# Optimization experiments

Hardware: AMD Instinct MI355X
Metric: run time of the kernel (lower is better)

## Reference

```python
import jax, jax.numpy as jnp
import numpy as np

B, S, D, H = 2, 2048, 1024, 16
HD = D // H


def setup_inputs() -> dict:
    key = jax.random.key(0)
    ks = jax.random.split(key, 9)
    s = 1.0 / np.sqrt(D)
    inp = {
        "x": jax.random.normal(ks[0], (B, S, D), dtype=jnp.float32),
        "Wq": jax.random.uniform(ks[1], (D, D), jnp.float32, -s, s),
        "bq": jax.random.uniform(ks[2], (D,), jnp.float32, -s, s),
        "Wk": jax.random.uniform(ks[3], (D, D), jnp.float32, -s, s),
        "bk": jax.random.uniform(ks[4], (D,), jnp.float32, -s, s),
        "Wv": jax.random.uniform(ks[5], (D, D), jnp.float32, -s, s),
        "bv": jax.random.uniform(ks[6], (D,), jnp.float32, -s, s),
        "Wo": jax.random.uniform(ks[7], (D, D), jnp.float32, -s, s),
        "bo": jax.random.uniform(ks[8], (D,), jnp.float32, -s, s),
    }
    return inp


def reference(x, Wq, bq, Wk, bk, Wv, bv, Wo, bo):
    # Linear projections (torch Linear: y = x @ W.T + b)
    q = x @ Wq.T + bq  # [B,S,D]
    k = x @ Wk.T + bk
    v = x @ Wv.T + bv
    # split heads -> [B,H,S,HD]
    q = q.reshape(B, S, H, HD).transpose(0, 2, 1, 3)
    k = k.reshape(B, S, H, HD).transpose(0, 2, 1, 3)
    v = v.reshape(B, S, H, HD).transpose(0, 2, 1, 3)
    scores = jnp.einsum('bhqd,bhkd->bhqk', q, k) / jnp.sqrt(jnp.float32(HD))
    attn = jax.nn.softmax(scores, axis=-1)
    o = jnp.einsum('bhqk,bhkd->bhqd', attn, v)  # [B,H,S,HD]
    o = o.transpose(0, 2, 1, 3).reshape(B, S, D)
    return o @ Wo.T + bo
```

## Files before the change

### kernel.cpp

```cpp
#include <hip/hip_runtime.h>
#include <hip/hip_bf16.h>
#include <stdint.h>


typedef __attribute__((ext_vector_type(8))) short bf16x8;
typedef __attribute__((ext_vector_type(4))) float f32x4;
typedef __attribute__((ext_vector_type(4))) float floatx4;
typedef __attribute__((ext_vector_type(4))) short shortx4;

#define MFMA16(a, b, c) __builtin_amdgcn_mfma_f32_16x16x32_bf16((a), (b), (c), 0, 0, 0)

static __device__ __forceinline__ short f2bf(float f) {
  __hip_bfloat16 h = __float2bfloat16(f);
  return *reinterpret_cast<short*>(&h);
}

static __device__ __forceinline__ uint32_t pack_bf16(float a, float b) {
  return (uint32_t)(uint16_t)f2bf(a) | ((uint32_t)(uint16_t)f2bf(b) << 16);
}

static __device__ __forceinline__ float fexp2(float x) {
#if __has_builtin(__builtin_amdgcn_exp2f)
  return __builtin_amdgcn_exp2f(x);
#else
  return exp2f(x);
#endif
}

static __device__ __forceinline__ void gload_lds16(const void* g, void* l) {
  __builtin_amdgcn_global_load_lds(
      (__attribute__((address_space(1))) void*)(void*)g,
      (__attribute__((address_space(3))) void*)l, 16, 0, 0);
}

__global__ void convert_kernel(const float* __restrict__ x,
                               const float* __restrict__ Wq, const float* __restrict__ Wk,
                               const float* __restrict__ Wv, const float* __restrict__ Wo,
                               const float* __restrict__ bq, const float* __restrict__ bk,
                               const float* __restrict__ bv,
                               __hip_bfloat16* __restrict__ xb,
                               __hip_bfloat16* __restrict__ wqkv,
                               __hip_bfloat16* __restrict__ wob,
                               float* __restrict__ bcat) {
  const int NX = (4096 * 1024) / 4;
  const int NW = (1024 * 1024) / 4;
  const int total = NX + 4 * NW;
  for (long i = (long)blockIdx.x * blockDim.x + threadIdx.x; i < total + 768;
       i += (long)gridDim.x * blockDim.x) {
    if (i < total) {
      const float* src;
      __hip_bfloat16* dst;
      long off;
      if (i < NX)             { src = x;  dst = xb;                       off = i; }
      else if (i < NX + NW)   { src = Wq; dst = wqkv;                     off = i - NX; }
      else if (i < NX + 2*NW) { src = Wk; dst = wqkv + 1024 * 1024;       off = i - NX - NW; }
      else if (i < NX + 3*NW) { src = Wv; dst = wqkv + 2 * 1024 * 1024;   off = i - NX - 2*NW; }
      else                    { src = Wo; dst = wob;                      off = i - NX - 3*NW; }
      floatx4 v = *(const floatx4*)(src + off * 4);
      shortx4 sv;
      sv.x = f2bf(v.x); sv.y = f2bf(v.y); sv.z = f2bf(v.z); sv.w = f2bf(v.w);
      *(shortx4*)(dst + off * 4) = sv;
    } else {
      int j = (int)(i - total);
#pragma unroll
      for (int u = 0; u < 4; ++u) {
        int n = j * 4 + u;
        float b = (n < 1024) ? bq[n] : (n < 2048 ? bk[n - 1024] : bv[n - 2048]);
        bcat[n] = b;
      }
    }
  }
}

template <bool OUT_BF16>
__global__ __launch_bounds__(256, 2) void gemm_bt(const __hip_bfloat16* __restrict__ A,
                                                  const __hip_bfloat16* __restrict__ Bm,
                                                  const float* __restrict__ bias,
                                                  void* __restrict__ Cout, int M, int N, int K,
                                                  float scale, int scale_limit) {
  __shared__ __hip_bfloat16 As[128 * 64];
  __shared__ __hip_bfloat16 Bs[128 * 64];
  const int tid = threadIdx.x;
  const int lane = tid & 63;
  const int w = tid >> 6;
  const int wm = w >> 1, wn = w & 1;

  const int nwg = gridDim.x;
  const int bi = blockIdx.x;
  const int wg = (bi & 7) * (nwg >> 3) + (bi >> 3);
  const int MT = M >> 7;
  const int tm = wg % MT, tn = wg / MT;
  const long brow = (long)tm * 128, bcol = (long)tn * 128;

  const int srow = tid >> 3;
  const int scsw = (tid & 7) << 4;

  f32x4 acc[4][4] = {};

  char* lAs = (char*)As + (tid & 0xC0) * 16;
  char* lBs = (char*)Bs + (tid & 0xC0) * 16;

  for (int k0 = 0; k0 < K; k0 += 64) {
#pragma unroll
    for (int p = 0; p < 4; ++p) {
      int r = p * 32 + srow;
      int cb = scsw ^ ((r & 7) << 4);
      gload_lds16(A + (brow + r) * (long)K + k0 + (cb >> 1), lAs + p * 4096);
      gload_lds16(Bm + (bcol + r) * (long)K + k0 + (cb >> 1), lBs + p * 4096);
    }
    __syncthreads();
#pragma unroll
    for (int ks = 0; ks < 2; ++ks) {
      bf16x8 af[4], bfr[4];
      const int cbase = ks * 64 + ((lane >> 4) << 4);
#pragma unroll
      for (int m = 0; m < 4; ++m) {
        int r = wm * 64 + m * 16 + (lane & 15);
        af[m] = *(const bf16x8*)((const char*)As + r * 128 + (cbase ^ ((r & 7) << 4)));
      }
#pragma unroll
      for (int n = 0; n < 4; ++n) {
        int r = wn * 64 + n * 16 + (lane & 15);
        bfr[n] = *(const bf16x8*)((const char*)Bs + r * 128 + (cbase ^ ((r & 7) << 4)));
      }
#pragma unroll
      for (int m = 0; m < 4; ++m)
#pragma unroll
        for (int n = 0; n < 4; ++n) acc[m][n] = MFMA16(af[m], bfr[n], acc[m][n]);
    }
    __syncthreads();
  }

#pragma unroll
  for (int n = 0; n < 4; ++n) {
    const long col = bcol + wn * 64 + n * 16 + (lane & 15);
    const float bv = bias[col];
    const float sc = (col < scale_limit) ? scale : 1.0f;
#pragma unroll
    for (int m = 0; m < 4; ++m) {
      const long row0 = brow + wm * 64 + m * 16 + ((lane >> 4) << 2);
#pragma unroll
      for (int j = 0; j < 4; ++j) {
        float v = (acc[m][n][j] + bv) * sc;
        if (OUT_BF16)
          ((__hip_bfloat16*)Cout)[(row0 + j) * N + col] = __float2bfloat16(v);
        else
          ((float*)Cout)[(row0 + j) * N + col] = v;
      }
    }
  }
}

__global__ __launch_bounds__(256, 2) void attn_kernel(const __hip_bfloat16* __restrict__ qkv,
                                                      __hip_bfloat16* __restrict__ O) {
  __shared__ __hip_bfloat16 Ks[2][128 * 64];
  __shared__ __hip_bfloat16 Vt[2][64 * 128];

  const int tid = threadIdx.x;
  const int lane = tid & 63;
  const int w = tid >> 6;
  const int g = lane >> 4;
  const int t = lane & 15;
  const int bi = blockIdx.x;
  const int qt = bi & 15, hh = (bi >> 4) & 15, bb = bi >> 8;
  const long rowQ0 = (long)bb * 2048 + qt * 128;
  const long rowK0 = (long)bb * 2048;
  const int qcol = hh * 64, kcol = 1024 + hh * 64, vcol = 2048 + hh * 64;

  bf16x8 qf[2][2];
#pragma unroll
  for (int m = 0; m < 2; ++m)
#pragma unroll
    for (int ks = 0; ks < 2; ++ks) {
      long r = rowQ0 + w * 32 + m * 16 + t;
      int c = qcol + ks * 32 + g * 8;
      qf[m][ks] = *(const bf16x8*)(qkv + r * 3072 + c);
    }

  f32x4 acc_o[2][4] = {};
  float mrun[2] = {-1e30f, -1e30f}, lrun[2] = {0.f, 0.f};
  uint32_t cpk[2][8][2];

  const int sb = (lane & 48) | ((lane & 48) >> 2);

  const int srow = tid >> 3;
  const int scsw = (tid & 7) << 4;
  const int vr = tid >> 1;
  const int vc0 = (tid & 1) * 32;
  const int vphib = 4 * (vr >> 5) + ((vr >> 2) & 3);
  const int vinb = ((vr >> 4) & 1) * 8 + (vr & 3) * 2;

  bf16x8 vreg[4];

#pragma unroll
  for (int p = 0; p < 4; ++p) {
    int r = p * 32 + srow;
    int cb = scsw ^ ((r & 7) << 4);
    gload_lds16(qkv + (rowK0 + r) * 3072 + kcol + (cb >> 1),
                (char*)(&Ks[0][0]) + (tid & 0xC0) * 16 + p * 4096);
  }
#pragma unroll
  for (int u = 0; u < 4; ++u)
    vreg[u] = *(const bf16x8*)(qkv + (rowK0 + vr) * 3072 + vcol + vc0 + u * 8);
#pragma unroll
  for (int u = 0; u < 4; ++u)
#pragma unroll
    for (int e = 0; e < 8; ++e) {
      int d = vc0 + u * 8 + e;
      *(short*)((char*)(&Vt[0][0]) + d * 256 + ((vphib ^ (d & 15)) << 4) + vinb) = vreg[u][e];
    }
  __syncthreads();

  int cur = 0;
  for (int tt = 0; tt < 16; ++tt) {
    if (tt < 15) {
      const long kvn = (long)(tt + 1) * 128;
#pragma unroll
      for (int p = 0; p < 4; ++p) {
        int r = p * 32 + srow;
        int cb = scsw ^ ((r & 7) << 4);
        gload_lds16(qkv + (rowK0 + kvn + r) * 3072 + kcol + (cb >> 1),
                    (char*)(&Ks[cur ^ 1][0]) + (tid & 0xC0) * 16 + p * 4096);
      }
#pragma unroll
      for (int u = 0; u < 4; ++u)
        vreg[u] = *(const bf16x8*)(qkv + (rowK0 + kvn + vr) * 3072 + vcol + vc0 + u * 8);
    }

    const char* KsCur = (const char*)(&Ks[cur][0]);
    const char* VtCur = (const char*)(&Vt[cur][0]);

    f32x4 s[2][8] = {};
#pragma unroll
    for (int ks = 0; ks < 2; ++ks) {
      const int cbase = ks * 64 + g * 16;
#pragma unroll
      for (int n = 0; n < 8; ++n) {
        const int r = n * 16 + t;
        const bf16x8 kf = *(const bf16x8*)(KsCur + r * 128 + (cbase ^ ((r & 7) << 4)));
        s[0][n] = MFMA16(kf, qf[0][ks], s[0][n]);
        s[1][n] = MFMA16(kf, qf[1][ks], s[1][n]);
      }
    }

#pragma unroll
    for (int m = 0; m < 2; ++m) {
      float mx = s[m][0][0];
#pragma unroll
      for (int n = 0; n < 8; ++n)
#pragma unroll
        for (int j = 0; j < 4; ++j) mx = fmaxf(mx, s[m][n][j]);
      mx = fmaxf(mx, __shfl_xor(mx, 16));
      mx = fmaxf(mx, __shfl_xor(mx, 32));
      const float newm = fmaxf(mrun[m], mx);
      const float corr = fexp2(mrun[m] - newm);
      mrun[m] = newm;
      float rs = 0.f;
#pragma unroll
      for (int n = 0; n < 8; ++n)
#pragma unroll
        for (int j = 0; j < 4; ++j) {
          float p = fexp2(s[m][n][j] - newm);
          s[m][n][j] = p;
          rs += p;
        }
      rs += __shfl_xor(rs, 16);
      rs += __shfl_xor(rs, 32);
      lrun[m] = lrun[m] * corr + rs;
#pragma unroll
      for (int j = 0; j < 4; ++j) {
        float cj = __shfl(corr, sb | j);
#pragma unroll
        for (int nd = 0; nd < 4; ++nd) acc_o[m][nd][j] *= cj;
      }
#pragma unroll
      for (int n = 0; n < 8; ++n) {
        cpk[m][n][0] = pack_bf16(s[m][n][0], s[m][n][1]);
        cpk[m][n][1] = pack_bf16(s[m][n][2], s[m][n][3]);
      }
    }

#pragma unroll
    for (int ks = 0; ks < 4; ++ks) {
      bf16x8 vf[4];
#pragma unroll
      for (int nd = 0; nd < 4; ++nd) {
        int d = nd * 16 + t;
        vf[nd] = *(const bf16x8*)(VtCur + d * 256 + (((4 * ks + g) ^ t) << 4));
      }
#pragma unroll
      for (int m = 0; m < 2; ++m) {
        union { bf16x8 v; uint32_t u[4]; } au;
        au.u[0] = cpk[m][2 * ks][0];
        au.u[1] = cpk[m][2 * ks][1];
        au.u[2] = cpk[m][2 * ks + 1][0];
        au.u[3] = cpk[m][2 * ks + 1][1];
#pragma unroll
        for (int nd = 0; nd < 4; ++nd) acc_o[m][nd] = MFMA16(au.v, vf[nd], acc_o[m][nd]);
      }
    }

    if (tt < 15) {
      char* VtNxt = (char*)(&Vt[cur ^ 1][0]);
#pragma unroll
      for (int u = 0; u < 4; ++u)
#pragma unroll
        for (int e = 0; e < 8; ++e) {
          int d = vc0 + u * 8 + e;
          *(short*)(VtNxt + d * 256 + ((vphib ^ (d & 15)) << 4) + vinb) = vreg[u][e];
        }
      __syncthreads();
      cur ^= 1;
    }
  }

#pragma unroll
  for (int m = 0; m < 2; ++m) {
    const float inv = 1.0f / lrun[m];
#pragma unroll
    for (int j = 0; j < 4; ++j) {
      const float ij = __shfl(inv, sb | j);
      const long r = rowQ0 + w * 32 + m * 16 + g * 4 + j;
#pragma unroll
      for (int nd = 0; nd < 4; ++nd) {
        O[r * 1024 + qcol + nd * 16 + t] = __float2bfloat16(acc_o[m][nd][j] * ij);
      }
    }
  }
}

extern "C" void kernel_launch(void* const* d_in, const int* in_sizes, int n_in,
                              void* d_out, int out_size, void* d_ws, size_t ws_size,
                              hipStream_t stream) {
  const float* x  = (const float*)d_in[0];
  const float* Wq = (const float*)d_in[1];
  const float* bq = (const float*)d_in[2];
  const float* Wk = (const float*)d_in[3];
  const float* bk = (const float*)d_in[4];
  const float* Wv = (const float*)d_in[5];
  const float* bv = (const float*)d_in[6];
  const float* Wo = (const float*)d_in[7];
  const float* bo = (const float*)d_in[8];

  __hip_bfloat16* ws = (__hip_bfloat16*)d_ws;
  __hip_bfloat16* xb   = ws;
  __hip_bfloat16* wqkv = xb + (size_t)4096 * 1024;
  __hip_bfloat16* wob  = wqkv + (size_t)3072 * 1024;
  __hip_bfloat16* qkvb = wob + (size_t)1024 * 1024;
  __hip_bfloat16* ob   = qkvb + (size_t)4096 * 3072;
  float* bcat = (float*)(ob + (size_t)4096 * 1024);

  const float qscale = 0.18033688011112042f;

  convert_kernel<<<dim3(2048), dim3(256), 0, stream>>>(x, Wq, Wk, Wv, Wo, bq, bk, bv,
                                                       xb, wqkv, wob, bcat);
  gemm_bt<true><<<dim3(768), dim3(256), 0, stream>>>(xb, wqkv, bcat, (void*)qkvb,
                                                     4096, 3072, 1024, qscale, 1024);
  attn_kernel<<<dim3(512), dim3(256), 0, stream>>>(qkvb, ob);
  gemm_bt<false><<<dim3(256), dim3(256), 0, stream>>>(ob, wob, bo, d_out,
                                                      4096, 1024, 1024, 1.0f, 0);
}
```

Baseline: 200.3 us.

## Split attention KV range across two wave groups and merge partial softmax results

The attention block grows to 512 threads. Two groups of four waves each process half of the key/value sequence for the same 128 query rows. The partial outputs and running max/sum are then merged through shared memory with a log-sum-exp combine. The intent is more waves per CU and half the serial KV loop length per wave. In exchange it drops the double-buffered prefetch, so each tile is loaded synchronously with two barriers per iteration. It also adds a merge step through LDS and raises the register pressure limit via launch bounds (512,4).

```diff
diff --git a/kernel.cpp b/kernel.cpp
--- a/kernel.cpp
+++ b/kernel.cpp
@@ -151,28 +151,33 @@
   }
 }
 
-__global__ __launch_bounds__(256, 2) void attn_kernel(const __hip_bfloat16* __restrict__ qkv,
+__global__ __launch_bounds__(512, 4) void attn_kernel(const __hip_bfloat16* __restrict__ qkv,
                                                       __hip_bfloat16* __restrict__ O) {
-  __shared__ __hip_bfloat16 Ks[2][128 * 64];
-  __shared__ __hip_bfloat16 Vt[2][64 * 128];
+  __shared__ char smem[65536];
 
   const int tid = threadIdx.x;
   const int lane = tid & 63;
-  const int w = tid >> 6;
+  const int wq = (tid >> 6) & 3;
+  const int grp = tid >> 8;
   const int g = lane >> 4;
   const int t = lane & 15;
+  const int gtid = tid & 255;
+
   const int bi = blockIdx.x;
   const int qt = bi & 15, hh = (bi >> 4) & 15, bb = bi >> 8;
   const long rowQ0 = (long)bb * 2048 + qt * 128;
-  const long rowK0 = (long)bb * 2048;
+  const long rowKg = (long)bb * 2048 + grp * 1024;
   const int qcol = hh * 64, kcol = 1024 + hh * 64, vcol = 2048 + hh * 64;
 
+  char* KsG = smem + grp * 16384;
+  char* VtG = smem + 32768 + grp * 16384;
+
   bf16x8 qf[2][2];
 #pragma unroll
   for (int m = 0; m < 2; ++m)
 #pragma unroll
     for (int ks = 0; ks < 2; ++ks) {
-      long r = rowQ0 + w * 32 + m * 16 + t;
+      long r = rowQ0 + wq * 32 + m * 16 + t;
       int c = qcol + ks * 32 + g * 8;
       qf[m][ks] = *(const bf16x8*)(qkv + r * 3072 + c);
     }
@@ -183,52 +188,32 @@
 
   const int sb = (lane & 48) | ((lane & 48) >> 2);
 
-  const int srow = tid >> 3;
-  const int scsw = (tid & 7) << 4;
-  const int vr = tid >> 1;
-  const int vc0 = (tid & 1) * 32;
+  const int srow = gtid >> 3;
+  const int scsw = (gtid & 7) << 4;
+  char* lK = KsG + (gtid & 0xC0) * 16;
+  const int vr = gtid >> 1;
+  const int vc0 = (gtid & 1) * 32;
   const int vphib = 4 * (vr >> 5) + ((vr >> 2) & 3);
   const int vinb = ((vr >> 4) & 1) * 8 + (vr & 3) * 2;
 
-  bf16x8 vreg[4];
-
-#pragma unroll
-  for (int p = 0; p < 4; ++p) {
-    int r = p * 32 + srow;
-    int cb = scsw ^ ((r & 7) << 4);
-    gload_lds16(qkv + (rowK0 + r) * 3072 + kcol + (cb >> 1),
-                (char*)(&Ks[0][0]) + (tid & 0xC0) * 16 + p * 4096);
-  }
-#pragma unroll
-  for (int u = 0; u < 4; ++u)
-    vreg[u] = *(const bf16x8*)(qkv + (rowK0 + vr) * 3072 + vcol + vc0 + u * 8);
-#pragma unroll
-  for (int u = 0; u < 4; ++u)
-#pragma unroll
-    for (int e = 0; e < 8; ++e) {
-      int d = vc0 + u * 8 + e;
-      *(short*)((char*)(&Vt[0][0]) + d * 256 + ((vphib ^ (d & 15)) << 4) + vinb) = vreg[u][e];
-    }
-  __syncthreads();
-
-  int cur = 0;
-  for (int tt = 0; tt < 16; ++tt) {
-    if (tt < 15) {
-      const long kvn = (long)(tt + 1) * 128;
-#pragma unroll
-      for (int p = 0; p < 4; ++p) {
-        int r = p * 32 + srow;
-        int cb = scsw ^ ((r & 7) << 4);
-        gload_lds16(qkv + (rowK0 + kvn + r) * 3072 + kcol + (cb >> 1),
-                    (char*)(&Ks[cur ^ 1][0]) + (tid & 0xC0) * 16 + p * 4096);
-      }
-#pragma unroll
-      for (int u = 0; u < 4; ++u)
-        vreg[u] = *(const bf16x8*)(qkv + (rowK0 + kvn + vr) * 3072 + vcol + vc0 + u * 8);
-    }
-
-    const char* KsCur = (const char*)(&Ks[cur][0]);
-    const char* VtCur = (const char*)(&Vt[cur][0]);
+  for (int tt = 0; tt < 8; ++tt) {
+    const long kv0 = rowKg + tt * 128;
+#pragma unroll
+    for (int p = 0; p < 4; ++p) {
+      int r = p * 32 + srow;
+      int cb = scsw ^ ((r & 7) << 4);
+      gload_lds16(qkv + (kv0 + r) * 3072 + kcol + (cb >> 1), lK + p * 4096);
+    }
+#pragma unroll
+    for (int u = 0; u < 4; ++u) {
+      bf16x8 v = *(const bf16x8*)(qkv + (kv0 + vr) * 3072 + vcol + vc0 + u * 8);
+#pragma unroll
+      for (int e = 0; e < 8; ++e) {
+        int d = vc0 + u * 8 + e;
+        *(short*)(VtG + d * 256 + ((vphib ^ (d & 15)) << 4) + vinb) = v[e];
+      }
+    }
+    __syncthreads();
 
     f32x4 s[2][8] = {};
 #pragma unroll
@@ -237,7 +222,7 @@
 #pragma unroll
       for (int n = 0; n < 8; ++n) {
         const int r = n * 16 + t;
-        const bf16x8 kf = *(const bf16x8*)(KsCur + r * 128 + (cbase ^ ((r & 7) << 4)));
+        const bf16x8 kf = *(const bf16x8*)(KsG + r * 128 + (cbase ^ ((r & 7) << 4)));
         s[0][n] = MFMA16(kf, qf[0][ks], s[0][n]);
         s[1][n] = MFMA16(kf, qf[1][ks], s[1][n]);
       }
@@ -286,7 +271,7 @@
 #pragma unroll
       for (int nd = 0; nd < 4; ++nd) {
         int d = nd * 16 + t;
-        vf[nd] = *(const bf16x8*)(VtCur + d * 256 + (((4 * ks + g) ^ t) << 4));
+        vf[nd] = *(const bf16x8*)(VtG + d * 256 + (((4 * ks + g) ^ t) << 4));
       }
 #pragma unroll
       for (int m = 0; m < 2; ++m) {
@@ -299,31 +284,49 @@
         for (int nd = 0; nd < 4; ++nd) acc_o[m][nd] = MFMA16(au.v, vf[nd], acc_o[m][nd]);
       }
     }
-
-    if (tt < 15) {
-      char* VtNxt = (char*)(&Vt[cur ^ 1][0]);
-#pragma unroll
-      for (int u = 0; u < 4; ++u)
-#pragma unroll
-        for (int e = 0; e < 8; ++e) {
-          int d = vc0 + u * 8 + e;
-          *(short*)(VtNxt + d * 256 + ((vphib ^ (d & 15)) << 4) + vinb) = vreg[u][e];
+    __syncthreads();
+  }
+
+  float* Opart = (float*)smem;
+  float* Ml = (float*)(smem + 32768);
+  if (grp == 1) {
+#pragma unroll
+    for (int m = 0; m < 2; ++m) {
+#pragma unroll
+      for (int nd = 0; nd < 4; ++nd)
+#pragma unroll
+        for (int j = 0; j < 4; ++j)
+          Opart[(wq * 32 + m * 16 + 4 * g + j) * 64 + nd * 16 + t] = acc_o[m][nd][j];
+      if (g == 0) {
+        int q = wq * 32 + m * 16 + t;
+        Ml[q * 2] = mrun[m];
+        Ml[q * 2 + 1] = lrun[m];
+      }
+    }
+  }
+  __syncthreads();
+  if (grp == 0) {
+#pragma unroll
+    for (int m = 0; m < 2; ++m) {
+      const int q = wq * 32 + m * 16 + t;
+      const float m1 = Ml[q * 2];
+      const float l1 = Ml[q * 2 + 1];
+      const float M = fmaxf(mrun[m], m1);
+      const float f0 = fexp2(mrun[m] - M);
+      const float f1 = fexp2(m1 - M);
+      const float inv = 1.0f / (lrun[m] * f0 + l1 * f1);
+#pragma unroll
+      for (int j = 0; j < 4; ++j) {
+        const float f0j = __shfl(f0, sb | j);
+        const float f1j = __shfl(f1, sb | j);
+        const float ivj = __shfl(inv, sb | j);
+        const int ql = wq * 32 + m * 16 + 4 * g + j;
+        const long r = rowQ0 + ql;
+#pragma unroll
+        for (int nd = 0; nd < 4; ++nd) {
+          float o = (acc_o[m][nd][j] * f0j + Opart[ql * 64 + nd * 16 + t] * f1j) * ivj;
+          O[r * 1024 + qcol + nd * 16 + t] = __float2bfloat16(o);
         }
-      __syncthreads();
-      cur ^= 1;
-    }
-  }
-
-#pragma unroll
-  for (int m = 0; m < 2; ++m) {
-    const float inv = 1.0f / lrun[m];
-#pragma unroll
-    for (int j = 0; j < 4; ++j) {
-      const float ij = __shfl(inv, sb | j);
-      const long r = rowQ0 + w * 32 + m * 16 + g * 4 + j;
-#pragma unroll
-      for (int nd = 0; nd < 4; ++nd) {
-        O[r * 1024 + qcol + nd * 16 + t] = __float2bfloat16(acc_o[m][nd][j] * ij);
       }
     }
   }
@@ -356,7 +359,7 @@
                                                        xb, wqkv, wob, bcat);
   gemm_bt<true><<<dim3(768), dim3(256), 0, stream>>>(xb, wqkv, bcat, (void*)qkvb,
                                                      4096, 3072, 1024, qscale, 1024);
-  attn_kernel<<<dim3(512), dim3(256), 0, stream>>>(qkvb, ob);
+  attn_kernel<<<dim3(512), dim3(512), 0, stream>>>(qkvb, ob);
   gemm_bt<false><<<dim3(256), dim3(256), 0, stream>>>(ob, wob, bo, d_out,
                                                       4096, 1024, 1024, 1.0f, 0);
 }
```

Result: slower. 347.5 us (+73.5%).
